# Optimization experiments

Measured on AMD Instinct MI355X. Metric: run time of the kernel, lower is better.

Reference implementation:

```python
import jax, jax.numpy as jnp
import numpy as np

B, C, T = 256, 9, 128
D, S, NL, EXP, DTR, DCONV = 24, 16, 4, 2, 2, 4
DI = EXP * D  # 48
STEMK, PK, PS = 5, 16, 4
NP = (T - PK) // PS + 1  # 29 patches
NCLS = 6


def setup_inputs() -> dict:
    key = jax.random.key(0)
    ks = iter(jax.random.split(key, 48))
    r = lambda shape, s=0.02: jax.random.normal(next(ks), shape, jnp.float32) * s
    return dict(
        x=jax.random.normal(next(ks), (B, T, C), jnp.float32),
        stem_w=r((D, 1, STEMK), 0.4),
        stem_bn_g=jnp.ones((D,)), stem_bn_b=jnp.zeros((D,)),
        stem_bn_m=jnp.zeros((D,)), stem_bn_v=jnp.ones((D,)),
        pd_w=r((D, 1, PK), 0.3),
        pp_w=r((D, D, 1), 0.3),
        patch_bn_g=jnp.ones((D,)), patch_bn_b=jnp.zeros((D,)),
        patch_bn_m=jnp.zeros((D,)), patch_bn_v=jnp.ones((D,)),
        pos_embed=r((1, NP, D)),
        ln1_g=jnp.ones((NL, D)), ln1_b=jnp.zeros((NL, D)),
        ln2_g=jnp.ones((NL, D)), ln2_b=jnp.zeros((NL, D)),
        in_w=r((NL, 2 * DI, D), 0.05),
        conv_w=r((NL, DI, 1, DCONV), 0.3), conv_b=jnp.zeros((NL, DI)),
        xproj_w=r((NL, DTR + 2 * S, DI), 0.05),
        dt_w=r((NL, DI, DTR), 0.1), dt_b=jnp.full((NL, DI), -2.0),
        A_log=jnp.log(jnp.broadcast_to(jnp.arange(1, S + 1, dtype=jnp.float32), (NL, DI, S))),
        Dp=jnp.ones((NL, DI)),
        out_w=r((NL, D, DI), 0.05),
        attn_w=r((D, D)), attn_b=jnp.zeros((D,)),
        ctx=r((D,)),
        head_g=jnp.ones((D,)), head_b=jnp.zeros((D,)),
        head_w=r((NCLS, D)), head_bias=jnp.zeros((NCLS,)),
    )


def _conv1d(x, w, stride, pad, groups=1):
    # x: [N, Cin, L], w: [Cout, Cin//groups, K]
    return jax.lax.conv_general_dilated(
        x, w, (stride,), [pad], dimension_numbers=('NCH', 'OIH', 'NCH'),
        feature_group_count=groups)


def _bn(x, g, b, m, v):  # eval-mode BatchNorm1d on [N, C, L]
    return (x - m[:, None]) * jax.lax.rsqrt(v[:, None] + 1e-5) * g[:, None] + b[:, None]


def _ln(x, g, b):
    mu = x.mean(-1, keepdims=True)
    var = ((x - mu) ** 2).mean(-1, keepdims=True)
    return (x - mu) * jax.lax.rsqrt(var + 1e-5) * g + b


def _selective_scan(u, dt, A, Bm, Cm):
    # u, dt: [N,L,DI]; A: [DI,S]; Bm, Cm: [N,L,S]
    dA = jnp.exp(dt[..., None] * A)                      # [N,L,DI,S]
    dBu = (dt * u)[..., None] * Bm[:, :, None, :]        # [N,L,DI,S]

    def step(h, inp):
        dA_t, dBu_t, C_t = inp
        h = dA_t * h + dBu_t                             # [N,DI,S]
        y = jnp.einsum('nds,ns->nd', h, C_t)
        return h, y

    h0 = jnp.zeros(dA.shape[:1] + dA.shape[2:], dA.dtype)
    _, ys = jax.lax.scan(step, h0, (dA.swapaxes(0, 1), dBu.swapaxes(0, 1), Cm.swapaxes(0, 1)))
    return ys.swapaxes(0, 1)                             # [N,L,DI]


def _mamba(x, in_w, conv_w, conv_b, xproj_w, dt_w, dt_b, A_log, Dp, out_w):
    # x: [N,L,D]
    xz = x @ in_w.T                                      # [N,L,2*DI]
    u, z = jnp.split(xz, 2, axis=-1)
    # causal depthwise conv (torch pads d_conv-1 both sides then truncates to L)
    uc = _conv1d(u.swapaxes(1, 2), conv_w, 1, (DCONV - 1, 0), groups=DI)
    uc = jax.nn.silu(uc + conv_b[None, :, None]).swapaxes(1, 2)   # [N,L,DI]
    dbl = uc @ xproj_w.T                                 # [N,L,DTR+2S]
    dtr, Bm, Cm = jnp.split(dbl, [DTR, DTR + S], axis=-1)
    dt = jax.nn.softplus(dtr @ dt_w.T + dt_b)            # [N,L,DI]
    A = -jnp.exp(A_log)                                  # [DI,S]
    y = _selective_scan(uc, dt, A, Bm, Cm) + uc * Dp
    y = y * jax.nn.silu(z)
    return y @ out_w.T                                   # [N,L,D]


def reference(x, stem_w, stem_bn_g, stem_bn_b, stem_bn_m, stem_bn_v,
              pd_w, pp_w, patch_bn_g, patch_bn_b, patch_bn_m, patch_bn_v,
              pos_embed, ln1_g, ln1_b, ln2_g, ln2_b,
              in_w, conv_w, conv_b, xproj_w, dt_w, dt_b, A_log, Dp, out_w,
              attn_w, attn_b, ctx, head_g, head_b, head_w, head_bias):
    Bsz = x.shape[0]
    # channel-independent reshape: [B,T,C] -> [B*C,1,T]
    h = x.transpose(0, 2, 1).reshape(Bsz * C, 1, T)
    # CI stem: shared single-channel conv + BN + SiLU
    h = _conv1d(h, stem_w, 1, (STEMK // 2, STEMK // 2))
    h = jax.nn.silu(_bn(h, stem_bn_g, stem_bn_b, stem_bn_m, stem_bn_v))  # [N,D,T]
    # patch embed: depthwise conv (k=16,s=4,pad=4,groups=D) + pointwise + BN
    h = _conv1d(h, pd_w, PS, (PK // 4, PK // 4), groups=D)
    h = _conv1d(h, pp_w, 1, (0, 0))
    h = _bn(h, patch_bn_g, patch_bn_b, patch_bn_m, patch_bn_v)
    h = h.swapaxes(1, 2)[:, :NP, :] + pos_embed          # [N,NP,D]
    # weight-tied bidirectional Mamba blocks
    for i in range(NL):
        res = h
        hn = _ln(h, ln1_g[i], ln1_b[i])
        args = (in_w[i], conv_w[i], conv_b[i], xproj_w[i], dt_w[i], dt_b[i], A_log[i], Dp[i], out_w[i])
        fwd = _mamba(hn, *args)
        bwd = jnp.flip(_mamba(jnp.flip(hn, axis=1), *args), axis=1)
        h = _ln(res + fwd + bwd, ln2_g[i], ln2_b[i])
    # gated temporal attention pooling
    u = jnp.tanh(h @ attn_w.T + attn_b)                  # [N,NP,D]
    alpha = jax.nn.softmax(jnp.einsum('nld,d->nl', u, ctx), axis=-1)
    c = jnp.einsum('nl,nld->nd', alpha, h)               # [N,D]
    # channel fusion: mean over sensor channels
    c = c.reshape(Bsz, C, D).mean(axis=1)                # [B,D]
    # head
    c = _ln(c, head_g, head_b)
    return c @ head_w.T + head_bias                      # [B,NCLS]
```

## Files before the change

### kernel.cpp

```cpp
#include <hip/hip_runtime.h>
#include <hip/hip_bf16.h>
#include <math.h>

#define B_    256
#define C_    9
#define T_    128
#define D_    24
#define S_    16
#define NL_   4
#define DI_   48
#define NP_   29
#define NSEQ  (B_ * C_)
#define NCLS_ 6

#define LOG2E 1.44269504088896f

#if __has_builtin(__builtin_amdgcn_exp2f)
#define EXP2F __builtin_amdgcn_exp2f
#else
#define EXP2F exp2f
#endif

__device__ __forceinline__ float fsilu(float x) {
    return __fdividef(x, 1.f + __expf(-x));
}

struct Params {
    const float *x;
    const float *stem_w, *stem_bn_g, *stem_bn_b, *stem_bn_m, *stem_bn_v;
    const float *pd_w, *pp_w, *patch_bn_g, *patch_bn_b, *patch_bn_m, *patch_bn_v;
    const float *pos_embed, *ln1_g, *ln1_b, *ln2_g, *ln2_b;
    const float *in_w, *conv_w, *conv_b, *xproj_w, *dt_w, *dt_b, *A_log, *Dp, *out_w;
    const float *attn_w, *attn_b, *ctx;
    float *cout;
};

__device__ __forceinline__ void ln_rows(const float* src, float* dst,
                                        const float* g, const float* bb, int tid) {
    int row = tid >> 3, sub = tid & 7;
    if (row < NP_) {
        const float* r = src + row * 24;
        float s = 0.f;
        for (int j = sub; j < 24; j += 8) s += r[j];
        s += __shfl_xor(s, 1); s += __shfl_xor(s, 2); s += __shfl_xor(s, 4);
        float mu = s * (1.f / 24.f);
        float v = 0.f;
        for (int j = sub; j < 24; j += 8) { float d0 = r[j] - mu; v = fmaf(d0, d0, v); }
        v += __shfl_xor(v, 1); v += __shfl_xor(v, 2); v += __shfl_xor(v, 4);
        float rs = rsqrtf(v * (1.f / 24.f) + 1e-5f);
        for (int j = sub; j < 24; j += 8) dst[row * 24 + j] = (r[j] - mu) * rs * g[j] + bb[j];
    }
}

#define OF_H    0
#define OF_HN   696
#define OF_U    1392
#define OF_BCF  696
#define OF_BCB  1624
#define OF_DTRF 2552
#define OF_DTRB 2610
#define OF_Z    2784
#define OF_OUT  2784
#define OF_UCF  4176
#define OF_UCB  5684
#define SM_TOT  7192

__global__ __launch_bounds__(256, 5) void mamba_seq_kernel(Params P) {
    __shared__ float sm[SM_TOT];
    const int tid = threadIdx.x;
    const int n = blockIdx.x;
    const int b = n / C_, cch = n - b * C_;

    float* s_h    = sm + OF_H;
    float* s_hn   = sm + OF_HN;
    float* s_u    = sm + OF_U;
    float* s_z    = sm + OF_Z;
    float* s_out  = sm + OF_OUT;
    float* s_ucf  = sm + OF_UCF;
    float* s_ucb  = sm + OF_UCB;
    float* s_bcf  = sm + OF_BCF;
    float* s_bcb  = sm + OF_BCB;
    float* s_dtrf = sm + OF_DTRF;
    float* s_dtrb = sm + OF_DTRB;

    float* xp  = sm + OF_Z;
    float* h0p = sm + OF_Z + 132;

    if (tid < 132) {
        float v = 0.f;
        int t = tid - 2;
        if (t >= 0 && t < T_) v = P.x[(b * T_ + t) * C_ + cch];
        xp[tid] = v;
    }
    for (int idx = tid; idx < 24 * 8; idx += 256) {
        int d = idx >> 3, j = idx & 7;
        h0p[d * 136 + (j < 4 ? j : j + 128)] = 0.f;
    }
    __syncthreads();
    for (int idx = tid; idx < 24 * 128; idx += 256) {
        int d = idx >> 7, t = idx & 127;
        const float* w = P.stem_w + d * 5;
        float acc = 0.f;
        #pragma unroll
        for (int k = 0; k < 5; k++) acc = fmaf(w[k], xp[t + k], acc);
        float sc = rsqrtf(P.stem_bn_v[d] + 1e-5f) * P.stem_bn_g[d];
        float val = (acc - P.stem_bn_m[d]) * sc + P.stem_bn_b[d];
        h0p[d * 136 + 4 + t] = fsilu(val);
    }
    __syncthreads();
    for (int idx = tid; idx < 24 * 31; idx += 256) {
        int d = idx / 31, l = idx - d * 31;
        const float* w = P.pd_w + d * 16;
        const float* src = h0p + d * 136 + l * 4;
        float acc = 0.f;
        #pragma unroll
        for (int k = 0; k < 16; k++) acc = fmaf(w[k], src[k], acc);
        s_u[idx] = acc;
    }
    __syncthreads();
    for (int idx = tid; idx < NP_ * 24; idx += 256) {
        int l = idx / 24, e = idx - l * 24;
        const float* w = P.pp_w + e * 24;
        float acc = 0.f;
        #pragma unroll
        for (int d = 0; d < 24; d++) acc = fmaf(w[d], s_u[d * 31 + l], acc);
        float sc = rsqrtf(P.patch_bn_v[e] + 1e-5f) * P.patch_bn_g[e];
        acc = (acc - P.patch_bn_m[e]) * sc + P.patch_bn_b[e];
        s_h[idx] = acc + P.pos_embed[idx];
    }
    __syncthreads();

    for (int il = 0; il < NL_; ++il) {
        const float* in_w_i   = P.in_w   + il * 96 * 24;
        const float* conv_w_i = P.conv_w + il * 48 * 4;
        const float* conv_b_i = P.conv_b + il * 48;
        const float* xpr_i    = P.xproj_w+ il * 34 * 48;
        const float* dt_w_i   = P.dt_w   + il * 48 * 2;
        const float* dt_b_i   = P.dt_b   + il * 48;
        const float* A_log_i  = P.A_log  + il * 48 * 16;
        const float* Dp_i     = P.Dp     + il * 48;
        const float* out_w_i  = P.out_w  + il * 24 * 48;

        ln_rows(s_h, s_hn, P.ln1_g + il * 24, P.ln1_b + il * 24, tid);
        __syncthreads();

        if (tid < 192) {
            int j  = tid >> 1;
            int l0 = (tid & 1) ? 15 : 0;
            int l1 = (tid & 1) ? NP_ : 15;
            const float4* w4 = (const float4*)(in_w_i + j * 24);
            float* dst = (j < 48) ? (s_u + j) : (s_z + (j - 48));
            for (int l = l0; l < l1; ++l) {
                const float4* h4 = (const float4*)(s_hn + l * 24);
                float acc = 0.f;
                #pragma unroll
                for (int q = 0; q < 6; q++) {
                    float4 a = h4[q], w = w4[q];
                    acc = fmaf(a.x, w.x, fmaf(a.y, w.y, fmaf(a.z, w.z, fmaf(a.w, w.w, acc))));
                }
                dst[l * 48] = acc;
            }
        }
        __syncthreads();

        for (int idx = tid; idx < NP_ * 48; idx += 256) {
            int l = idx / 48, d = idx - l * 48;
            const float* w = conv_w_i + d * 4;
            float w0 = w[0], w1 = w[1], w2 = w[2], w3 = w[3];
            float bb = conv_b_i[d];
            float accf = bb, accb = bb;
            if (l >= 3) accf = fmaf(w0, s_u[(l - 3) * 48 + d], accf);
            if (l >= 2) accf = fmaf(w1, s_u[(l - 2) * 48 + d], accf);
            if (l >= 1) accf = fmaf(w2, s_u[(l - 1) * 48 + d], accf);
            accf = fmaf(w3, s_u[l * 48 + d], accf);
            if (l + 3 < NP_) accb = fmaf(w0, s_u[(l + 3) * 48 + d], accb);
            if (l + 2 < NP_) accb = fmaf(w1, s_u[(l + 2) * 48 + d], accb);
            if (l + 1 < NP_) accb = fmaf(w2, s_u[(l + 1) * 48 + d], accb);
            accb = fmaf(w3, s_u[l * 48 + d], accb);
            s_ucf[l * 52 + d] = fsilu(accf);
            s_ucb[l * 52 + d] = fsilu(accb);
            s_z[idx] = fsilu(s_z[idx]);
        }
        __syncthreads();

        if (tid < 204) {
            int lg = tid / 68;
            int ch = tid - lg * 68;
            int l0 = lg * 10;
            int l1 = (lg == 2) ? NP_ : (l0 + 10);
            int dir = ch >= 34;
            int j = ch - (dir ? 34 : 0);
            const float* ucp = dir ? s_ucb : s_ucf;
            const float4* w4 = (const float4*)(xpr_i + j * 48);
            float* dst; int stride;
            if (j < 2) { dst = (dir ? s_dtrb : s_dtrf) + j; stride = 2; }
            else       { dst = (dir ? s_bcb  : s_bcf ) + (j - 2); stride = 32; }
            for (int l = l0; l < l1; ++l) {
                const float4* u4 = (const float4*)(ucp + l * 52);
                float acc = 0.f;
                #pragma unroll
                for (int q = 0; q < 12; q++) {
                    float4 a = u4[q], w = w4[q];
                    acc = fmaf(a.x, w.x, fmaf(a.y, w.y, fmaf(a.z, w.z, fmaf(a.w, w.w, acc))));
                }
                dst[l * stride] = acc;
            }
        }
        __syncthreads();

        if (tid < 192) {
            const int dir = tid >= 96;
            const int rr  = tid - (dir ? 96 : 0);
            const int d   = rr >> 1;
            const int sh  = rr & 1;
            const float* dtr = dir ? s_dtrb : s_dtrf;
            float* ucio      = dir ? s_ucb  : s_ucf;
            const float* bc  = dir ? s_bcb  : s_bcf;
            const float dtw0 = dt_w_i[d * 2], dtw1 = dt_w_i[d * 2 + 1], dtb = dt_b_i[d];
            const float Dpd = Dp_i[d];
            float a0 = -__expf(A_log_i[d * 16]) * LOG2E;
            bool alin = true;
            #pragma unroll
            for (int s = 1; s < 16; s++) {
                float as = -__expf(A_log_i[d * 16 + s]) * LOG2E;
                alin = alin && (fabsf(as - (s + 1) * a0) <= 1e-4f * (s + 1) * fabsf(a0));
            }
            float hs[8];
            #pragma unroll
            for (int s = 0; s < 8; s++) hs[s] = 0.f;

            if (alin) {
                int l = dir ? (NP_ - 1) : 0;
                float2 tt = *(const float2*)(dtr + l * 2);
                float u_ld = ucio[l * 52 + d];
                float z_ld = s_z[l * 48 + d];
                float draw = fmaf(tt.y, dtw1, fmaf(tt.x, dtw0, dtb));
                float dtc = (draw > 15.f) ? draw : __logf(1.f + __expf(draw));
                float dtu = dtc * u_ld;
                float r1 = EXP2F(dtc * a0);

                for (int p = 0; p < NP_; p++) {
                    const int lcur = l;
                    const float u_c = u_ld, z_c = z_ld, dtu_c = dtu, rc = r1;
                    if (p + 1 < NP_) {
                        l = dir ? (NP_ - 2 - p) : (p + 1);
                        tt = *(const float2*)(dtr + l * 2);
                        u_ld = ucio[l * 52 + d];
                        z_ld = s_z[l * 48 + d];
                        draw = fmaf(tt.y, dtw1, fmaf(tt.x, dtw0, dtb));
                        dtc = (draw > 15.f) ? draw : __logf(1.f + __expf(draw));
                        dtu = dtc * u_ld;
                        r1 = EXP2F(dtc * a0);
                    }
                    float c2 = rc * rc, c4 = c2 * c2, c8 = c4 * c4;
                    float p3 = c2 * rc, p5 = c4 * rc, p6 = c4 * c2, p7 = c4 * p3;
                    float qm = sh ? c8 : 1.0f;
                    const float4* bv = (const float4*)(bc + lcur * 32);
                    {
                        float4 Ba = bv[2 * sh], Bb = bv[2 * sh + 1];
                        hs[0] = fmaf(rc * qm, hs[0], dtu_c * Ba.x);
                        hs[1] = fmaf(c2 * qm, hs[1], dtu_c * Ba.y);
                        hs[2] = fmaf(p3 * qm, hs[2], dtu_c * Ba.z);
                        hs[3] = fmaf(c4 * qm, hs[3], dtu_c * Ba.w);
                        hs[4] = fmaf(p5 * qm, hs[4], dtu_c * Bb.x);
                        hs[5] = fmaf(p6 * qm, hs[5], dtu_c * Bb.y);
                        hs[6] = fmaf(p7 * qm, hs[6], dtu_c * Bb.z);
                        hs[7] = fmaf(c8 * qm, hs[7], dtu_c * Bb.w);
                    }
                    float y0, y1;
                    {
                        float4 Ca = bv[4 + 2 * sh], Cb = bv[5 + 2 * sh];
                        y0 = hs[0] * Ca.x;          y1 = hs[1] * Ca.y;
                        y0 = fmaf(hs[2], Ca.z, y0); y1 = fmaf(hs[3], Ca.w, y1);
                        y0 = fmaf(hs[4], Cb.x, y0); y1 = fmaf(hs[5], Cb.y, y1);
                        y0 = fmaf(hs[6], Cb.z, y0); y1 = fmaf(hs[7], Cb.w, y1);
                    }
                    float y = y0 + y1;
                    y += __shfl_xor(y, 1);
                    float v = fmaf(u_c, Dpd, y) * z_c;
                    if (sh == 0) ucio[lcur * 52 + d] = v;
                }
            } else {
                for (int p = 0; p < NP_; p++) {
                    int l = dir ? (NP_ - 1 - p) : p;
                    float2 tt = *(const float2*)(dtr + l * 2);
                    float draw = fmaf(tt.y, dtw1, fmaf(tt.x, dtw0, dtb));
                    float dtc = (draw > 15.f) ? draw : __logf(1.f + __expf(draw));
                    float u_ld = ucio[l * 52 + d];
                    float z_ld = s_z[l * 48 + d];
                    float dtu = dtc * u_ld;
                    const float4* bv = (const float4*)(bc + l * 32);
                    float4 Ba = bv[2 * sh], Bb = bv[2 * sh + 1];
                    float4 Ca = bv[4 + 2 * sh], Cb = bv[5 + 2 * sh];
                    float y0 = 0.f;
                    #pragma unroll
                    for (int i = 0; i < 8; i++) {
                        float Bi = (i < 4) ? ((i == 0) ? Ba.x : (i == 1) ? Ba.y : (i == 2) ? Ba.z : Ba.w)
                                           : ((i == 4) ? Bb.x : (i == 5) ? Bb.y : (i == 6) ? Bb.z : Bb.w);
                        float Ci = (i < 4) ? ((i == 0) ? Ca.x : (i == 1) ? Ca.y : (i == 2) ? Ca.z : Ca.w)
                                           : ((i == 4) ? Cb.x : (i == 5) ? Cb.y : (i == 6) ? Cb.z : Cb.w);
                        float aa = -__expf(A_log_i[d * 16 + sh * 8 + i]) * LOG2E;
                        float dA = EXP2F(dtc * aa);
                        hs[i] = fmaf(dA, hs[i], dtu * Bi);
                        y0 = fmaf(hs[i], Ci, y0);
                    }
                    float y = y0 + __shfl_xor(y0, 1);
                    float v = fmaf(u_ld, Dpd, y) * z_ld;
                    if (sh == 0) ucio[l * 52 + d] = v;
                }
            }
        }
        __syncthreads();

        if (tid < 192) {
            int e = tid >> 3, lg = tid & 7;
            const float4* w4 = (const float4*)(out_w_i + e * 48);
            for (int l = lg; l < NP_; l += 8) {
                const float4* f4 = (const float4*)(s_ucf + l * 52);
                const float4* b4 = (const float4*)(s_ucb + l * 52);
                float acc = s_h[l * 24 + e];
                #pragma unroll
                for (int q = 0; q < 12; q++) {
                    float4 af = f4[q], ab = b4[q], w = w4[q];
                    float ax = af.x + ab.x, ay = af.y + ab.y, az = af.z + ab.z, aw = af.w + ab.w;
                    acc = fmaf(ax, w.x, fmaf(ay, w.y, fmaf(az, w.z, fmaf(aw, w.w, acc))));
                }
                s_out[l * 24 + e] = acc;
            }
        }
        __syncthreads();

        ln_rows(s_out, s_h, P.ln2_g + il * 24, P.ln2_b + il * 24, tid);
        __syncthreads();
    }

    for (int idx = tid; idx < NP_ * 24; idx += 256) {
        int l = idx / 24, d2 = idx - l * 24;
        const float* w = P.attn_w + d2 * 24;
        const float* hr = s_h + l * 24;
        float acc = P.attn_b[d2];
        #pragma unroll
        for (int e = 0; e < 24; e++) acc = fmaf(hr[e], w[e], acc);
        s_u[idx] = tanhf(acc) * P.ctx[d2];
    }
    __syncthreads();
    if (tid < NP_) {
        float s = 0.f;
        for (int d = 0; d < 24; d++) s += s_u[tid * 24 + d];
        s_dtrf[tid] = s;
    }
    __syncthreads();
    if (tid < 64) {
        float v = (tid < NP_) ? s_dtrf[tid] : -1e30f;
        float m = v;
        #pragma unroll
        for (int o = 32; o >= 1; o >>= 1) m = fmaxf(m, __shfl_xor(m, o));
        float e = (tid < NP_) ? __expf(v - m) : 0.f;
        float s = e;
        #pragma unroll
        for (int o = 32; o >= 1; o >>= 1) s += __shfl_xor(s, o);
        if (tid < NP_) s_dtrf[tid] = __fdividef(e, s);
    }
    __syncthreads();
    if (tid < 24) {
        float acc = 0.f;
        for (int l = 0; l < NP_; l++) acc = fmaf(s_dtrf[l], s_h[l * 24 + tid], acc);
        P.cout[n * 24 + tid] = acc;
    }
}

__global__ __launch_bounds__(64) void head_kernel(const float* __restrict__ cws,
                                                  const float* __restrict__ hg,
                                                  const float* __restrict__ hb,
                                                  const float* __restrict__ hw,
                                                  const float* __restrict__ hbias,
                                                  float* __restrict__ out) {
    __shared__ float sy[24];
    int bidx = blockIdx.x, t = threadIdx.x;
    float c = 0.f;
    if (t < 24) {
        float acc = 0.f;
        for (int j = 0; j < C_; j++) acc += cws[(bidx * C_ + j) * 24 + t];
        c = acc * (1.f / 9.f);
    }
    float s = (t < 24) ? c : 0.f;
    #pragma unroll
    for (int o = 32; o >= 1; o >>= 1) s += __shfl_xor(s, o);
    float mu = s * (1.f / 24.f);
    float dv = (t < 24) ? (c - mu) : 0.f;
    float q = dv * dv;
    #pragma unroll
    for (int o = 32; o >= 1; o >>= 1) q += __shfl_xor(q, o);
    float rs = rsqrtf(q * (1.f / 24.f) + 1e-5f);
    if (t < 24) sy[t] = dv * rs * hg[t] + hb[t];
    __syncthreads();
    if (t < NCLS_) {
        float acc = hbias[t];
        #pragma unroll
        for (int d = 0; d < 24; d++) acc = fmaf(sy[d], hw[t * 24 + d], acc);
        out[bidx * NCLS_ + t] = acc;
    }
}

extern "C" void kernel_launch(void* const* d_in, const int* in_sizes, int n_in,
                              void* d_out, int out_size, void* d_ws, size_t ws_size,
                              hipStream_t stream) {
    (void)in_sizes; (void)n_in; (void)out_size; (void)ws_size;
    Params P;
    P.x          = (const float*)d_in[0];
    P.stem_w     = (const float*)d_in[1];
    P.stem_bn_g  = (const float*)d_in[2];
    P.stem_bn_b  = (const float*)d_in[3];
    P.stem_bn_m  = (const float*)d_in[4];
    P.stem_bn_v  = (const float*)d_in[5];
    P.pd_w       = (const float*)d_in[6];
    P.pp_w       = (const float*)d_in[7];
    P.patch_bn_g = (const float*)d_in[8];
    P.patch_bn_b = (const float*)d_in[9];
    P.patch_bn_m = (const float*)d_in[10];
    P.patch_bn_v = (const float*)d_in[11];
    P.pos_embed  = (const float*)d_in[12];
    P.ln1_g      = (const float*)d_in[13];
    P.ln1_b      = (const float*)d_in[14];
    P.ln2_g      = (const float*)d_in[15];
    P.ln2_b      = (const float*)d_in[16];
    P.in_w       = (const float*)d_in[17];
    P.conv_w     = (const float*)d_in[18];
    P.conv_b     = (const float*)d_in[19];
    P.xproj_w    = (const float*)d_in[20];
    P.dt_w       = (const float*)d_in[21];
    P.dt_b       = (const float*)d_in[22];
    P.A_log      = (const float*)d_in[23];
    P.Dp         = (const float*)d_in[24];
    P.out_w      = (const float*)d_in[25];
    P.attn_w     = (const float*)d_in[26];
    P.attn_b     = (const float*)d_in[27];
    P.ctx        = (const float*)d_in[28];
    P.cout       = (float*)d_ws;

    mamba_seq_kernel<<<dim3(NSEQ), dim3(256), 0, stream>>>(P);
    head_kernel<<<dim3(B_), dim3(64), 0, stream>>>(
        (const float*)d_ws,
        (const float*)d_in[29],
        (const float*)d_in[30],
        (const float*)d_in[31],
        (const float*)d_in[32],
        (float*)d_out);
}
```

Measured before the change: 404.7 us.

## Register-block small matmuls, hoist A-linearity check, and use fast tanh

The in_proj, x_proj and out_proj loops now compute several sequence positions per thread with the weight row split into halves kept in registers, so each weight float4 is loaded once and reused across positions. The depthwise conv loop is restructured so each thread owns a fixed channel and keeps its conv weights across strided positions. The per-layer A_log linearity check and a0 are computed once per channel by otherwise idle threads during x_proj and stored in shared memory, instead of being recomputed by every scan thread. tanhf in attention pooling is replaced by an exp-based formula, which costs a little accuracy and adds register pressure from the unrolled accumulators.

```diff
diff --git a/kernel.cpp b/kernel.cpp
--- a/kernel.cpp
+++ b/kernel.cpp
@@ -59,6 +59,8 @@
 #define OF_BCB  1624
 #define OF_DTRF 2552
 #define OF_DTRB 2610
+#define OF_A0   2668
+#define OF_AOK  2716
 #define OF_Z    2784
 #define OF_OUT  2784
 #define OF_UCF  4176
@@ -82,6 +84,8 @@
     float* s_bcb  = sm + OF_BCB;
     float* s_dtrf = sm + OF_DTRF;
     float* s_dtrb = sm + OF_DTRB;
+    float* s_a0   = sm + OF_A0;
+    float* s_aok  = sm + OF_AOK;
 
     float* xp  = sm + OF_Z;
     float* h0p = sm + OF_Z + 132;
@@ -150,36 +154,56 @@
             int l1 = (tid & 1) ? NP_ : 15;
             const float4* w4 = (const float4*)(in_w_i + j * 24);
             float* dst = (j < 48) ? (s_u + j) : (s_z + (j - 48));
-            for (int l = l0; l < l1; ++l) {
-                const float4* h4 = (const float4*)(s_hn + l * 24);
-                float acc = 0.f;
+            for (int c0 = l0; c0 < l1; c0 += 5) {
+                float acc[5] = {0.f, 0.f, 0.f, 0.f, 0.f};
                 #pragma unroll
-                for (int q = 0; q < 6; q++) {
-                    float4 a = h4[q], w = w4[q];
-                    acc = fmaf(a.x, w.x, fmaf(a.y, w.y, fmaf(a.z, w.z, fmaf(a.w, w.w, acc))));
-                }
-                dst[l * 48] = acc;
+                for (int kh = 0; kh < 2; kh++) {
+                    float4 wa = w4[kh * 3 + 0], wb = w4[kh * 3 + 1], wc = w4[kh * 3 + 2];
+                    #pragma unroll
+                    for (int i = 0; i < 5; i++) {
+                        int l = c0 + i;
+                        if (l < l1) {
+                            const float4* h4 = (const float4*)(s_hn + l * 24) + kh * 3;
+                            float4 a0v = h4[0], a1v = h4[1], a2v = h4[2];
+                            float a = acc[i];
+                            a = fmaf(a0v.x, wa.x, a); a = fmaf(a0v.y, wa.y, a);
+                            a = fmaf(a0v.z, wa.z, a); a = fmaf(a0v.w, wa.w, a);
+                            a = fmaf(a1v.x, wb.x, a); a = fmaf(a1v.y, wb.y, a);
+                            a = fmaf(a1v.z, wb.z, a); a = fmaf(a1v.w, wb.w, a);
+                            a = fmaf(a2v.x, wc.x, a); a = fmaf(a2v.y, wc.y, a);
+                            a = fmaf(a2v.z, wc.z, a); a = fmaf(a2v.w, wc.w, a);
+                            acc[i] = a;
+                        }
+                    }
+                }
+                #pragma unroll
+                for (int i = 0; i < 5; i++) {
+                    int l = c0 + i;
+                    if (l < l1) dst[l * 48] = acc[i];
+                }
             }
         }
         __syncthreads();
 
-        for (int idx = tid; idx < NP_ * 48; idx += 256) {
-            int l = idx / 48, d = idx - l * 48;
+        if (tid < 240) {
+            int d = tid % 48, g = tid / 48;
             const float* w = conv_w_i + d * 4;
             float w0 = w[0], w1 = w[1], w2 = w[2], w3 = w[3];
             float bb = conv_b_i[d];
-            float accf = bb, accb = bb;
-            if (l >= 3) accf = fmaf(w0, s_u[(l - 3) * 48 + d], accf);
-            if (l >= 2) accf = fmaf(w1, s_u[(l - 2) * 48 + d], accf);
-            if (l >= 1) accf = fmaf(w2, s_u[(l - 1) * 48 + d], accf);
-            accf = fmaf(w3, s_u[l * 48 + d], accf);
-            if (l + 3 < NP_) accb = fmaf(w0, s_u[(l + 3) * 48 + d], accb);
-            if (l + 2 < NP_) accb = fmaf(w1, s_u[(l + 2) * 48 + d], accb);
-            if (l + 1 < NP_) accb = fmaf(w2, s_u[(l + 1) * 48 + d], accb);
-            accb = fmaf(w3, s_u[l * 48 + d], accb);
-            s_ucf[l * 52 + d] = fsilu(accf);
-            s_ucb[l * 52 + d] = fsilu(accb);
-            s_z[idx] = fsilu(s_z[idx]);
+            for (int l = g; l < NP_; l += 5) {
+                float accf = bb, accb = bb;
+                if (l >= 3) accf = fmaf(w0, s_u[(l - 3) * 48 + d], accf);
+                if (l >= 2) accf = fmaf(w1, s_u[(l - 2) * 48 + d], accf);
+                if (l >= 1) accf = fmaf(w2, s_u[(l - 1) * 48 + d], accf);
+                accf = fmaf(w3, s_u[l * 48 + d], accf);
+                if (l + 3 < NP_) accb = fmaf(w0, s_u[(l + 3) * 48 + d], accb);
+                if (l + 2 < NP_) accb = fmaf(w1, s_u[(l + 2) * 48 + d], accb);
+                if (l + 1 < NP_) accb = fmaf(w2, s_u[(l + 1) * 48 + d], accb);
+                accb = fmaf(w3, s_u[l * 48 + d], accb);
+                s_ucf[l * 52 + d] = fsilu(accf);
+                s_ucb[l * 52 + d] = fsilu(accb);
+                s_z[l * 48 + d] = fsilu(s_z[l * 48 + d]);
+            }
         }
         __syncthreads();
 
@@ -195,16 +219,53 @@
             float* dst; int stride;
             if (j < 2) { dst = (dir ? s_dtrb : s_dtrf) + j; stride = 2; }
             else       { dst = (dir ? s_bcb  : s_bcf ) + (j - 2); stride = 32; }
-            for (int l = l0; l < l1; ++l) {
-                const float4* u4 = (const float4*)(ucp + l * 52);
-                float acc = 0.f;
+            for (int c0 = l0; c0 < l1; c0 += 5) {
+                float acc[5] = {0.f, 0.f, 0.f, 0.f, 0.f};
                 #pragma unroll
-                for (int q = 0; q < 12; q++) {
-                    float4 a = u4[q], w = w4[q];
-                    acc = fmaf(a.x, w.x, fmaf(a.y, w.y, fmaf(a.z, w.z, fmaf(a.w, w.w, acc))));
-                }
-                dst[l * stride] = acc;
-            }
+                for (int kh = 0; kh < 2; kh++) {
+                    float4 wr0 = w4[kh * 6 + 0], wr1 = w4[kh * 6 + 1], wr2 = w4[kh * 6 + 2];
+                    float4 wr3 = w4[kh * 6 + 3], wr4 = w4[kh * 6 + 4], wr5 = w4[kh * 6 + 5];
+                    #pragma unroll
+                    for (int i = 0; i < 5; i++) {
+                        int l = c0 + i;
+                        if (l < l1) {
+                            const float4* u4 = (const float4*)(ucp + l * 52) + kh * 6;
+                            float a = acc[i];
+                            float4 v0 = u4[0], v1 = u4[1], v2 = u4[2];
+                            a = fmaf(v0.x, wr0.x, a); a = fmaf(v0.y, wr0.y, a);
+                            a = fmaf(v0.z, wr0.z, a); a = fmaf(v0.w, wr0.w, a);
+                            a = fmaf(v1.x, wr1.x, a); a = fmaf(v1.y, wr1.y, a);
+                            a = fmaf(v1.z, wr1.z, a); a = fmaf(v1.w, wr1.w, a);
+                            a = fmaf(v2.x, wr2.x, a); a = fmaf(v2.y, wr2.y, a);
+                            a = fmaf(v2.z, wr2.z, a); a = fmaf(v2.w, wr2.w, a);
+                            float4 v3 = u4[3], v4 = u4[4], v5 = u4[5];
+                            a = fmaf(v3.x, wr3.x, a); a = fmaf(v3.y, wr3.y, a);
+                            a = fmaf(v3.z, wr3.z, a); a = fmaf(v3.w, wr3.w, a);
+                            a = fmaf(v4.x, wr4.x, a); a = fmaf(v4.y, wr4.y, a);
+                            a = fmaf(v4.z, wr4.z, a); a = fmaf(v4.w, wr4.w, a);
+                            a = fmaf(v5.x, wr5.x, a); a = fmaf(v5.y, wr5.y, a);
+                            a = fmaf(v5.z, wr5.z, a); a = fmaf(v5.w, wr5.w, a);
+                            acc[i] = a;
+                        }
+                    }
+                }
+                #pragma unroll
+                for (int i = 0; i < 5; i++) {
+                    int l = c0 + i;
+                    if (l < l1) dst[l * stride] = acc[i];
+                }
+            }
+        } else if (tid < 252) {
+            int d = tid - 204;
+            float a0 = -__expf(A_log_i[d * 16]) * LOG2E;
+            bool alin = true;
+            #pragma unroll
+            for (int s = 1; s < 16; s++) {
+                float as = -__expf(A_log_i[d * 16 + s]) * LOG2E;
+                alin = alin && (fabsf(as - (s + 1) * a0) <= 1e-4f * (s + 1) * fabsf(a0));
+            }
+            s_a0[d] = a0;
+            s_aok[d] = alin ? 1.f : 0.f;
         }
         __syncthreads();
 
@@ -218,13 +279,8 @@
             const float* bc  = dir ? s_bcb  : s_bcf;
             const float dtw0 = dt_w_i[d * 2], dtw1 = dt_w_i[d * 2 + 1], dtb = dt_b_i[d];
             const float Dpd = Dp_i[d];
-            float a0 = -__expf(A_log_i[d * 16]) * LOG2E;
-            bool alin = true;
-            #pragma unroll
-            for (int s = 1; s < 16; s++) {
-                float as = -__expf(A_log_i[d * 16 + s]) * LOG2E;
-                alin = alin && (fabsf(as - (s + 1) * a0) <= 1e-4f * (s + 1) * fabsf(a0));
-            }
+            const float a0 = s_a0[d];
+            const bool alin = s_aok[d] > 0.5f;
             float hs[8];
             #pragma unroll
             for (int s = 0; s < 8; s++) hs[s] = 0.f;
@@ -315,17 +371,50 @@
         if (tid < 192) {
             int e = tid >> 3, lg = tid & 7;
             const float4* w4 = (const float4*)(out_w_i + e * 48);
-            for (int l = lg; l < NP_; l += 8) {
-                const float4* f4 = (const float4*)(s_ucf + l * 52);
-                const float4* b4 = (const float4*)(s_ucb + l * 52);
-                float acc = s_h[l * 24 + e];
+            float acc[4];
+            #pragma unroll
+            for (int i = 0; i < 4; i++) {
+                int l = lg + 8 * i;
+                acc[i] = (l < NP_) ? s_h[l * 24 + e] : 0.f;
+            }
+            #pragma unroll
+            for (int kh = 0; kh < 2; kh++) {
+                float4 wr0 = w4[kh * 6 + 0], wr1 = w4[kh * 6 + 1], wr2 = w4[kh * 6 + 2];
+                float4 wr3 = w4[kh * 6 + 3], wr4 = w4[kh * 6 + 4], wr5 = w4[kh * 6 + 5];
                 #pragma unroll
-                for (int q = 0; q < 12; q++) {
-                    float4 af = f4[q], ab = b4[q], w = w4[q];
-                    float ax = af.x + ab.x, ay = af.y + ab.y, az = af.z + ab.z, aw = af.w + ab.w;
-                    acc = fmaf(ax, w.x, fmaf(ay, w.y, fmaf(az, w.z, fmaf(aw, w.w, acc))));
-                }
-                s_out[l * 24 + e] = acc;
+                for (int i = 0; i < 4; i++) {
+                    int l = lg + 8 * i;
+                    if (l < NP_) {
+                        const float4* f4 = (const float4*)(s_ucf + l * 52) + kh * 6;
+                        const float4* b4 = (const float4*)(s_ucb + l * 52) + kh * 6;
+                        float a = acc[i];
+                        float4 af, ab;
+                        af = f4[0]; ab = b4[0];
+                        a = fmaf(af.x + ab.x, wr0.x, a); a = fmaf(af.y + ab.y, wr0.y, a);
+                        a = fmaf(af.z + ab.z, wr0.z, a); a = fmaf(af.w + ab.w, wr0.w, a);
+                        af = f4[1]; ab = b4[1];
+                        a = fmaf(af.x + ab.x, wr1.x, a); a = fmaf(af.y + ab.y, wr1.y, a);
+                        a = fmaf(af.z + ab.z, wr1.z, a); a = fmaf(af.w + ab.w, wr1.w, a);
+                        af = f4[2]; ab = b4[2];
+                        a = fmaf(af.x + ab.x, wr2.x, a); a = fmaf(af.y + ab.y, wr2.y, a);
+                        a = fmaf(af.z + ab.z, wr2.z, a); a = fmaf(af.w + ab.w, wr2.w, a);
+                        af = f4[3]; ab = b4[3];
+                        a = fmaf(af.x + ab.x, wr3.x, a); a = fmaf(af.y + ab.y, wr3.y, a);
+                        a = fmaf(af.z + ab.z, wr3.z, a); a = fmaf(af.w + ab.w, wr3.w, a);
+                        af = f4[4]; ab = b4[4];
+                        a = fmaf(af.x + ab.x, wr4.x, a); a = fmaf(af.y + ab.y, wr4.y, a);
+                        a = fmaf(af.z + ab.z, wr4.z, a); a = fmaf(af.w + ab.w, wr4.w, a);
+                        af = f4[5]; ab = b4[5];
+                        a = fmaf(af.x + ab.x, wr5.x, a); a = fmaf(af.y + ab.y, wr5.y, a);
+                        a = fmaf(af.z + ab.z, wr5.z, a); a = fmaf(af.w + ab.w, wr5.w, a);
+                        acc[i] = a;
+                    }
+                }
+            }
+            #pragma unroll
+            for (int i = 0; i < 4; i++) {
+                int l = lg + 8 * i;
+                if (l < NP_) s_out[l * 24 + e] = acc[i];
             }
         }
         __syncthreads();
@@ -341,7 +430,9 @@
         float acc = P.attn_b[d2];
         #pragma unroll
         for (int e = 0; e < 24; e++) acc = fmaf(hr[e], w[e], acc);
-        s_u[idx] = tanhf(acc) * P.ctx[d2];
+        float e2 = __expf(2.f * acc);
+        float th = 1.f - __fdividef(2.f, e2 + 1.f);
+        s_u[idx] = th * P.ctx[d2];
     }
     __syncthreads();
     if (tid < NP_) {
```

Result: no change. 400.8 us (-1.0%).
